# Optimization experiments

Measured on AMD Instinct MI355X. Metric: run time of the kernel, lower is better.

## Reference

```python
import jax, jax.numpy as jnp
import numpy as np

EMBED = 1024
HEADS = 16
HEAD_DIM = EMBED // HEADS

def setup_inputs() -> dict:
    key = jax.random.key(0)
    ks = jax.random.split(key, 12)
    N, L, E = 4, 2048, EMBED
    s = 1.0 / np.sqrt(E)
    return {
        "values": jax.random.normal(ks[0], (N, L, E), jnp.float32),
        "keys": jax.random.normal(ks[1], (N, L, E), jnp.float32),
        "query": jax.random.normal(ks[2], (N, L, E), jnp.float32),
        "mask": jnp.ones((N, 1, 1, L), jnp.int32),
        "Wv": jax.random.normal(ks[3], (E, E), jnp.float32) * s,
        "bv": jnp.zeros((E,), jnp.float32),
        "Wk": jax.random.normal(ks[4], (E, E), jnp.float32) * s,
        "bk": jnp.zeros((E,), jnp.float32),
        "Wq": jax.random.normal(ks[5], (E, E), jnp.float32) * s,
        "bq": jnp.zeros((E,), jnp.float32),
        "Wo": jax.random.normal(ks[6], (E, E), jnp.float32) * s,
        "bo": jnp.zeros((E,), jnp.float32),
    }

def reference(values, keys, query, mask, Wv, bv, Wk, bk, Wq, bq, Wo, bo):
    N, L, E = values.shape
    H, D = HEADS, HEAD_DIM
    v = (values @ Wv + bv).reshape(N, L, H, D)
    k = (keys @ Wk + bk).reshape(N, L, H, D)
    q = (query @ Wq + bq).reshape(N, L, H, D)
    # energy: [N, H, Lq, Lk]
    energy = jnp.einsum('nqhd,nkhd->nhqk', q, k)
    energy = jnp.where(mask == 0, jnp.float32(-1e20), energy)
    attn = jax.nn.softmax(energy / np.sqrt(D), axis=3)
    out = jnp.einsum('nhqk,nkhd->nqhd', attn, v).reshape(N, L, E)
    return out @ Wo + bo
```

## Files before the change

kernel.cpp:

```cpp
#include <hip/hip_runtime.h>
#include <hip/hip_bf16.h>


#define N_B 4
#define L_S 2048
#define E_D 1024
#define H_N 16
#define D_H 64

typedef __attribute__((ext_vector_type(8))) short short8;
typedef __attribute__((ext_vector_type(8))) unsigned short ushort8;
typedef __attribute__((ext_vector_type(4))) unsigned short ushort4v;
typedef __attribute__((ext_vector_type(4))) float f32x4;

#define EXP2F(x) __builtin_amdgcn_exp2f(x)

__device__ __forceinline__ unsigned short f2b(float f) {
    unsigned int u = __builtin_bit_cast(unsigned int, f);
    u += 0x7fffu + ((u >> 16) & 1u);
    return (unsigned short)(u >> 16);
}

__device__ __forceinline__ void gload16(const void* g, void* l) {
    __builtin_amdgcn_global_load_lds(
        (const __attribute__((address_space(1))) void*)g,
        (__attribute__((address_space(3))) void*)l, 16, 0, 0);
}

__global__ __launch_bounds__(256) void cvt3_kernel(const float* __restrict__ v,
                                                   const float* __restrict__ k,
                                                   const float* __restrict__ q,
                                                   unsigned short* __restrict__ out) {
    int z = blockIdx.y;
    const float* in = (z == 0) ? v : ((z == 1) ? k : q);
    unsigned short* o = out + (size_t)z * (8u << 20);
    size_t i = (size_t)blockIdx.x * 256 + threadIdx.x;
    const float* p = in + i * 8;
    ushort8 ov;
#pragma unroll
    for (int j = 0; j < 8; j++) ov[j] = f2b(p[j]);
    *(ushort8*)(o + i * 8) = ov;
}

__global__ __launch_bounds__(256) void wtrans4_kernel(const float* __restrict__ W0,
                                                      const float* __restrict__ W1,
                                                      const float* __restrict__ W2,
                                                      const float* __restrict__ W3,
                                                      unsigned short* __restrict__ WtBase) {
    __shared__ float t[64][65];
    int z = blockIdx.z;
    const float* W = (z == 0) ? W0 : ((z == 1) ? W1 : ((z == 2) ? W2 : W3));
    unsigned short* Wt = WtBase + (size_t)z * (1u << 20);
    int bx = blockIdx.x, by = blockIdx.y;
    int tx = threadIdx.x;
    int r0 = tx >> 4;
    int c4 = (tx & 15) << 2;
#pragma unroll
    for (int rr = 0; rr < 64; rr += 16) {
        const float* src = W + (size_t)(by * 64 + rr + r0) * E_D + bx * 64 + c4;
        float4 v = *(const float4*)src;
        t[rr + r0][c4 + 0] = v.x; t[rr + r0][c4 + 1] = v.y;
        t[rr + r0][c4 + 2] = v.z; t[rr + r0][c4 + 3] = v.w;
    }
    __syncthreads();
#pragma unroll
    for (int rr = 0; rr < 64; rr += 16) {
        int nrow = bx * 64 + rr + r0;
        ushort4v o;
#pragma unroll
        for (int j = 0; j < 4; j++) o[j] = f2b(t[c4 + j][rr + r0]);
        *(ushort4v*)(Wt + (size_t)nrow * E_D + by * 64 + c4) = o;
    }
}

template <int OUTF32>
__device__ __forceinline__ void gemm_body(
    const unsigned short* __restrict__ A, const unsigned short* __restrict__ Bt,
    const float* __restrict__ bias, void* __restrict__ C,
    int K, int Nc, float scale,
    unsigned short* As, unsigned short* Bs, int n0, int m0) {
    int lane = threadIdx.x & 63, wave = threadIdx.x >> 6;
    int wr = (wave >> 1) * 64, wc = (wave & 1) * 64;
    f32x4 acc[4][4] = {};
    int nk = K >> 6;
    for (int kt = 0; kt < nk; ++kt) {
#pragma unroll
        for (int i = 0; i < 4; i++) {
            int c = (i * 4 + wave) * 64 + lane;
            int row = c >> 3;
            int csw = (c & 7) ^ (row & 7);
            gload16(A + (size_t)(m0 + row) * K + kt * 64 + csw * 8,
                    As + (size_t)(i * 4 + wave) * 512);
            gload16(Bt + (size_t)(n0 + row) * K + kt * 64 + csw * 8,
                    Bs + (size_t)(i * 4 + wave) * 512);
        }
        __syncthreads();
#pragma unroll
        for (int ks = 0; ks < 2; ++ks) {
            short8 a[4], b[4];
#pragma unroll
            for (int mi = 0; mi < 4; mi++) {
                int row = wr + mi * 16 + (lane & 15);
                int ch = (ks * 4 + (lane >> 4)) ^ (row & 7);
                a[mi] = *(const short8*)(As + row * 64 + ch * 8);
            }
#pragma unroll
            for (int ni = 0; ni < 4; ni++) {
                int col = wc + ni * 16 + (lane & 15);
                int ch = (ks * 4 + (lane >> 4)) ^ (col & 7);
                b[ni] = *(const short8*)(Bs + col * 64 + ch * 8);
            }
#pragma unroll
            for (int mi = 0; mi < 4; mi++)
#pragma unroll
                for (int ni = 0; ni < 4; ni++)
                    acc[mi][ni] = __builtin_amdgcn_mfma_f32_16x16x32_bf16(
                        a[mi], b[ni], acc[mi][ni], 0, 0, 0);
        }
        __syncthreads();
    }
#pragma unroll
    for (int ni = 0; ni < 4; ni++) {
        int col = n0 + wc + ni * 16 + (lane & 15);
        float bb = bias[col];
#pragma unroll
        for (int mi = 0; mi < 4; mi++) {
            int rbase = m0 + wr + mi * 16 + (lane >> 4) * 4;
#pragma unroll
            for (int r = 0; r < 4; r++) {
                float v = (acc[mi][ni][r] + bb) * scale;
                if (OUTF32)
                    ((float*)C)[(size_t)(rbase + r) * Nc + col] = v;
                else
                    ((unsigned short*)C)[(size_t)(rbase + r) * Nc + col] = f2b(v);
            }
        }
    }
}

template <int OUTF32>
__global__ __launch_bounds__(256, 3) void gemm_kernel(
    const unsigned short* __restrict__ A, const unsigned short* __restrict__ Bt,
    const float* __restrict__ bias, void* __restrict__ C,
    int M, int K, int Nc, float scale) {
    __shared__ unsigned short As[128 * 64];
    __shared__ unsigned short Bs[128 * 64];
    gemm_body<OUTF32>(A, Bt, bias, C, K, Nc, scale, As, Bs,
                      blockIdx.x * 128, blockIdx.y * 128);
}

__global__ __launch_bounds__(256, 3) void gemm3_kernel(
    const unsigned short* __restrict__ Abase, const unsigned short* __restrict__ Wtbase,
    const float* __restrict__ bv, const float* __restrict__ bk, const float* __restrict__ bq,
    unsigned short* __restrict__ Cbase, float qscale) {
    __shared__ unsigned short As[128 * 64];
    __shared__ unsigned short Bs[128 * 64];
    int z = blockIdx.z;
    const unsigned short* A  = Abase + (size_t)z * (8u << 20);
    const unsigned short* Bt = Wtbase + (size_t)z * (1u << 20);
    const float* bias = (z == 0) ? bv : ((z == 1) ? bk : bq);
    unsigned short* C = Cbase + (size_t)z * (8u << 20);
    float scale = (z == 2) ? qscale : 1.0f;
    gemm_body<0>(A, Bt, bias, C, E_D, E_D, scale, As, Bs,
                 blockIdx.x * 128, blockIdx.y * 128);
}

__global__ __launch_bounds__(256) void vtrans_kernel(const unsigned short* __restrict__ v,
                                                     unsigned short* __restrict__ vt) {
    __shared__ unsigned short t[64 * 65];
    int l0 = blockIdx.x * 64, h = blockIdx.y, n = blockIdx.z;
    int tx = threadIdx.x;
    int r = tx >> 3;
    int c8 = (tx & 7) << 3;
#pragma unroll
    for (int rr = 0; rr < 64; rr += 32) {
        ushort8 val = *(const ushort8*)(v + (size_t)(n * L_S + l0 + rr + r) * E_D + h * 64 + c8);
#pragma unroll
        for (int j = 0; j < 8; j++) t[(rr + r) * 65 + c8 + j] = val[j];
    }
    __syncthreads();
#pragma unroll
    for (int rr = 0; rr < 64; rr += 32) {
        int d = rr + r;
        ushort8 o;
#pragma unroll
        for (int j = 0; j < 8; j++) o[j] = t[(c8 + j) * 65 + d];
        *(ushort8*)(vt + (size_t)((n * H_N + h) * D_H + d) * L_S + l0 + c8) = o;
    }
}

__global__ __launch_bounds__(512, 4) void attn_kernel(
    const unsigned short* __restrict__ qb, const unsigned short* __restrict__ kb,
    const unsigned short* __restrict__ vt, const int* __restrict__ mask,
    unsigned short* __restrict__ aout) {
    __shared__ unsigned short Ks[2][64 * 64];
    __shared__ unsigned short Vs[2][64 * 64];
    __shared__ unsigned short Ps[8][32 * 64];
    __shared__ alignas(8) unsigned char okb[256];
    int lane = threadIdx.x & 63, wave = threadIdx.x >> 6;
    int g = lane >> 4, c = lane & 15;
    const float SHIFT = 20.0f;

    int bid = blockIdx.x;
    int xcd = bid & 7, idx = bid >> 3;
    int grp = xcd * 8 + (idx >> 3);
    int q0 = (idx & 7) * 256;
    int h = grp & 15;
    int n = grp >> 4;

    const unsigned short* qptr  = qb + (size_t)n * L_S * E_D + h * 64;
    const unsigned short* kbase = kb + (size_t)n * L_S * E_D + h * 64;
    const unsigned short* vbase = vt + (size_t)(n * H_N + h) * D_H * L_S;
    const int* mbase = mask + n * L_S;

    if (threadIdx.x < 256) {
        int t8 = threadIdx.x * 8;
        int4 ma = *(const int4*)(mbase + t8);
        int4 mb = *(const int4*)(mbase + t8 + 4);
        int ok = (ma.x != 0) & (ma.y != 0) & (ma.z != 0) & (ma.w != 0) &
                 (mb.x != 0) & (mb.y != 0) & (mb.z != 0) & (mb.w != 0);
        okb[threadIdx.x] = (unsigned char)ok;
    }
    unsigned short* Qs = &Ps[0][0];
#pragma unroll
    for (int i = 0; i < 4; i++) {
        int ci = i * 8 + wave;
        int cc = ci * 64 + lane;
        int row = cc >> 3, csw = (cc & 7) ^ (row & 7);
        gload16(qptr + (size_t)(q0 + row) * E_D + csw * 8, Qs + (size_t)ci * 512);
    }
    {
        int cc = wave * 64 + lane;
        int row = cc >> 3, csw = (cc & 7) ^ (row & 7);
        gload16(kbase + (size_t)row * E_D + csw * 8, Ks[0] + wave * 512);
        gload16(vbase + (size_t)row * L_S + csw * 8, Vs[0] + wave * 512);
    }
    __syncthreads();

    short8 qf[2][2];
#pragma unroll
    for (int m = 0; m < 2; m++)
#pragma unroll
        for (int kd = 0; kd < 2; kd++) {
            int row = wave * 32 + m * 16 + c;
            int ch = (kd * 4 + g) ^ (row & 7);
            qf[m][kd] = *(const short8*)(Qs + row * 64 + ch * 8);
        }

    f32x4 o[2][4] = {};
    float lrun[2] = {0.f, 0.f};
    unsigned short* pw = &Ps[wave][0];

    const int NT = L_S / 64;
    for (int kt = 0; kt < NT; ++kt) {
        int cur = kt & 1;
        if (kt + 1 < NT) {
            int cc = wave * 64 + lane;
            int row = cc >> 3, csw = (cc & 7) ^ (row & 7);
            gload16(kbase + (size_t)((kt + 1) * 64 + row) * E_D + csw * 8,
                    Ks[cur ^ 1] + wave * 512);
            gload16(vbase + (size_t)row * L_S + (kt + 1) * 64 + csw * 8,
                    Vs[cur ^ 1] + wave * 512);
            asm volatile("s_waitcnt vmcnt(2)" ::: "memory");
        } else {
            asm volatile("s_waitcnt vmcnt(0)" ::: "memory");
        }
        __builtin_amdgcn_s_barrier();
        __builtin_amdgcn_sched_barrier(0);

        const unsigned short* KsC = Ks[cur];
        const unsigned short* VsC = Vs[cur];

        f32x4 sT[2][4] = {};
        __builtin_amdgcn_s_setprio(1);
#pragma unroll
        for (int kd = 0; kd < 2; kd++)
#pragma unroll
            for (int kg = 0; kg < 4; kg++) {
                int krow = kg * 16 + c;
                int ch = (kd * 4 + g) ^ (krow & 7);
                short8 kf = *(const short8*)(KsC + krow * 64 + ch * 8);
                sT[0][kg] = __builtin_amdgcn_mfma_f32_16x16x32_bf16(kf, qf[0][kd], sT[0][kg], 0, 0, 0);
                sT[1][kg] = __builtin_amdgcn_mfma_f32_16x16x32_bf16(kf, qf[1][kd], sT[1][kg], 0, 0, 0);
            }
        __builtin_amdgcn_s_setprio(0);

        uint2 fl = *(const uint2*)&okb[kt * 8];
        bool dense = ((fl.x & fl.y) == 0x01010101u);
        if (!dense) {
#pragma unroll
            for (int kg = 0; kg < 4; kg++) {
                int4 mv = *(const int4*)(mbase + kt * 64 + kg * 16 + g * 4);
                float m0 = mv.x ? 0.f : -1e30f;
                float m1 = mv.y ? 0.f : -1e30f;
                float m2 = mv.z ? 0.f : -1e30f;
                float m3 = mv.w ? 0.f : -1e30f;
                sT[0][kg][0] += m0; sT[1][kg][0] += m0;
                sT[0][kg][1] += m1; sT[1][kg][1] += m1;
                sT[0][kg][2] += m2; sT[1][kg][2] += m2;
                sT[0][kg][3] += m3; sT[1][kg][3] += m3;
            }
        }
#pragma unroll
        for (int m = 0; m < 2; m++) {
            float ps = 0.f;
            int prow = m * 16 + c;
#pragma unroll
            for (int kg = 0; kg < 4; kg++) {
                float p0 = EXP2F(sT[m][kg][0] - SHIFT);
                float p1 = EXP2F(sT[m][kg][1] - SHIFT);
                float p2 = EXP2F(sT[m][kg][2] - SHIFT);
                float p3 = EXP2F(sT[m][kg][3] - SHIFT);
                ps += (p0 + p1) + (p2 + p3);
                unsigned int w0, w1;
                asm("v_cvt_pk_bf16_f32 %0, %1, %2" : "=v"(w0) : "v"(p0), "v"(p1));
                asm("v_cvt_pk_bf16_f32 %0, %1, %2" : "=v"(w1) : "v"(p2), "v"(p3));
                int c16 = kg * 2 + (g >> 1);
                int off = prow * 64 + ((c16 ^ (prow & 7)) << 3) + ((g & 1) << 2);
                uint2 wv; wv.x = w0; wv.y = w1;
                *(uint2*)(pw + off) = wv;
            }
            ps += __shfl_xor(ps, 16);
            ps += __shfl_xor(ps, 32);
            lrun[m] += ps;
        }
        __builtin_amdgcn_s_setprio(1);
#pragma unroll
        for (int kk = 0; kk < 2; kk++) {
            short8 pb[2];
#pragma unroll
            for (int m = 0; m < 2; m++) {
                int prow = m * 16 + c;
                int ch = (kk * 4 + g) ^ (prow & 7);
                pb[m] = *(const short8*)(pw + prow * 64 + ch * 8);
            }
#pragma unroll
            for (int dg = 0; dg < 4; dg++) {
                int drow = dg * 16 + c;
                int ch = (kk * 4 + g) ^ (drow & 7);
                short8 vb = *(const short8*)(VsC + drow * 64 + ch * 8);
                o[0][dg] = __builtin_amdgcn_mfma_f32_16x16x32_bf16(vb, pb[0], o[0][dg], 0, 0, 0);
                o[1][dg] = __builtin_amdgcn_mfma_f32_16x16x32_bf16(vb, pb[1], o[1][dg], 0, 0, 0);
            }
        }
        __builtin_amdgcn_s_setprio(0);
        asm volatile("s_waitcnt lgkmcnt(0)" ::: "memory");
        __builtin_amdgcn_s_barrier();
    }
#pragma unroll
    for (int m = 0; m < 2; m++) {
        float inv = 1.f / lrun[m];
        int row = q0 + wave * 32 + m * 16 + c;
#pragma unroll
        for (int dg = 0; dg < 4; dg++) {
            ushort4v ov;
#pragma unroll
            for (int r = 0; r < 4; r++) ov[r] = f2b(o[m][dg][r] * inv);
            *(ushort4v*)(aout + (size_t)(n * L_S + row) * E_D + h * 64 + dg * 16 + g * 4) = ov;
        }
    }
}

extern "C" void kernel_launch(void* const* d_in, const int* in_sizes, int n_in,
                              void* d_out, int out_size, void* d_ws, size_t ws_size,
                              hipStream_t stream) {
    const float* values = (const float*)d_in[0];
    const float* keys   = (const float*)d_in[1];
    const float* query  = (const float*)d_in[2];
    const int*   mask   = (const int*)d_in[3];
    const float* Wv = (const float*)d_in[4];  const float* bv = (const float*)d_in[5];
    const float* Wk = (const float*)d_in[6];  const float* bk = (const float*)d_in[7];
    const float* Wq = (const float*)d_in[8];  const float* bq = (const float*)d_in[9];
    const float* Wo = (const float*)d_in[10]; const float* bo = (const float*)d_in[11];
    float* out = (float*)d_out;
    char* ws = (char*)d_ws;
    const size_t MB = 1ull << 20;
    unsigned short* xv  = (unsigned short*)(ws + 0 * MB);
    unsigned short* wtv = (unsigned short*)(ws + 48 * MB);
    unsigned short* wto = (unsigned short*)(ws + 54 * MB);
    unsigned short* vbf = (unsigned short*)(ws + 56 * MB);
    unsigned short* kbf = (unsigned short*)(ws + 72 * MB);
    unsigned short* qbf = (unsigned short*)(ws + 88 * MB);
    unsigned short* vT  = (unsigned short*)(ws + 0 * MB);
    unsigned short* aob = (unsigned short*)(ws + 16 * MB);

    const float QS = 0.125f * 1.4426950408889634f;

    cvt3_kernel<<<dim3(4096, 3), 256, 0, stream>>>(values, keys, query, xv);
    wtrans4_kernel<<<dim3(16, 16, 4), 256, 0, stream>>>(Wv, Wk, Wq, Wo, wtv);
    gemm3_kernel<<<dim3(E_D / 128, (N_B * L_S) / 128, 3), 256, 0, stream>>>(
        xv, wtv, bv, bk, bq, vbf, QS);
    vtrans_kernel<<<dim3(32, 16, 4), 256, 0, stream>>>(vbf, vT);
    attn_kernel<<<dim3(512), 512, 0, stream>>>(qbf, kbf, vT, mask, aob);
    gemm_kernel<1><<<dim3(E_D / 128, (N_B * L_S) / 128), 256, 0, stream>>>(
        aob, wto, bo, out, N_B * L_S, E_D, E_D, 1.0f);
}
```

Measured before the change: 217.8 us.

## Fuse V transpose into V-projection GEMM epilogue via LDS staging

```diff
diff --git a/kernel.cpp b/kernel.cpp
--- a/kernel.cpp
+++ b/kernel.cpp
@@ -73,7 +73,7 @@
     }
 }
 
-template <int OUTF32>
+template <int OUTMODE>
 __device__ __forceinline__ void gemm_body(
     const unsigned short* __restrict__ A, const unsigned short* __restrict__ Bt,
     const float* __restrict__ bias, void* __restrict__ C,
@@ -119,6 +119,42 @@
         }
         __syncthreads();
     }
+    if (OUTMODE == 2) {
+        int g = lane >> 4, c = lane & 15;
+        unsigned short* tb = As + wave * 4096;
+#pragma unroll
+        for (int ni = 0; ni < 4; ni++) {
+            int cl = ni * 16 + c;
+            float bb = bias[n0 + wc + cl];
+#pragma unroll
+            for (int mi = 0; mi < 4; mi++) {
+#pragma unroll
+                for (int r = 0; r < 4; r++) {
+                    int rl = mi * 16 + g * 4 + r;
+                    tb[rl * 64 + (((cl >> 3) ^ (rl & 7)) << 3) + (cl & 7)] =
+                        f2b((acc[mi][ni][r] + bb) * scale);
+                }
+            }
+        }
+        int mrow = m0 + wr;
+        int n = mrow >> 11;
+        int l0 = mrow & 2047;
+        int h = (n0 + wc) >> 6;
+        unsigned short* vt = (unsigned short*)C;
+#pragma unroll
+        for (int i = 0; i < 8; i++) {
+            int d = i * 8 + (lane >> 3);
+            int lc = (lane & 7) * 8;
+            ushort8 ov;
+#pragma unroll
+            for (int j = 0; j < 8; j++) {
+                int rl = lc + j;
+                ov[j] = tb[rl * 64 + (((d >> 3) ^ (rl & 7)) << 3) + (d & 7)];
+            }
+            *(ushort8*)(vt + (size_t)((n * H_N + h) * D_H + d) * L_S + l0 + lc) = ov;
+        }
+        return;
+    }
 #pragma unroll
     for (int ni = 0; ni < 4; ni++) {
         int col = n0 + wc + ni * 16 + (lane & 15);
@@ -129,7 +165,7 @@
 #pragma unroll
             for (int r = 0; r < 4; r++) {
                 float v = (acc[mi][ni][r] + bb) * scale;
-                if (OUTF32)
+                if (OUTMODE == 1)
                     ((float*)C)[(size_t)(rbase + r) * Nc + col] = v;
                 else
                     ((unsigned short*)C)[(size_t)(rbase + r) * Nc + col] = f2b(v);
@@ -138,54 +174,32 @@
     }
 }
 
-template <int OUTF32>
-__global__ __launch_bounds__(256, 3) void gemm_kernel(
+template <int OUTMODE>
+__global__ __launch_bounds__(256, 2) void gemm_kernel(
     const unsigned short* __restrict__ A, const unsigned short* __restrict__ Bt,
     const float* __restrict__ bias, void* __restrict__ C,
     int M, int K, int Nc, float scale) {
-    __shared__ unsigned short As[128 * 64];
-    __shared__ unsigned short Bs[128 * 64];
-    gemm_body<OUTF32>(A, Bt, bias, C, K, Nc, scale, As, Bs,
-                      blockIdx.x * 128, blockIdx.y * 128);
-}
-
-__global__ __launch_bounds__(256, 3) void gemm3_kernel(
+    __shared__ unsigned short SMEM[2][128 * 64];
+    gemm_body<OUTMODE>(A, Bt, bias, C, K, Nc, scale, SMEM[0], SMEM[1],
+                       blockIdx.x * 128, blockIdx.y * 128);
+}
+
+__global__ __launch_bounds__(256, 2) void gemm3_kernel(
     const unsigned short* __restrict__ Abase, const unsigned short* __restrict__ Wtbase,
     const float* __restrict__ bv, const float* __restrict__ bk, const float* __restrict__ bq,
-    unsigned short* __restrict__ Cbase, float qscale) {
-    __shared__ unsigned short As[128 * 64];
-    __shared__ unsigned short Bs[128 * 64];
+    unsigned short* __restrict__ vT, unsigned short* __restrict__ kbf,
+    unsigned short* __restrict__ qbf, float qscale) {
+    __shared__ unsigned short SMEM[2][128 * 64];
     int z = blockIdx.z;
     const unsigned short* A  = Abase + (size_t)z * (8u << 20);
     const unsigned short* Bt = Wtbase + (size_t)z * (1u << 20);
-    const float* bias = (z == 0) ? bv : ((z == 1) ? bk : bq);
-    unsigned short* C = Cbase + (size_t)z * (8u << 20);
-    float scale = (z == 2) ? qscale : 1.0f;
-    gemm_body<0>(A, Bt, bias, C, E_D, E_D, scale, As, Bs,
-                 blockIdx.x * 128, blockIdx.y * 128);
-}
-
-__global__ __launch_bounds__(256) void vtrans_kernel(const unsigned short* __restrict__ v,
-                                                     unsigned short* __restrict__ vt) {
-    __shared__ unsigned short t[64 * 65];
-    int l0 = blockIdx.x * 64, h = blockIdx.y, n = blockIdx.z;
-    int tx = threadIdx.x;
-    int r = tx >> 3;
-    int c8 = (tx & 7) << 3;
-#pragma unroll
-    for (int rr = 0; rr < 64; rr += 32) {
-        ushort8 val = *(const ushort8*)(v + (size_t)(n * L_S + l0 + rr + r) * E_D + h * 64 + c8);
-#pragma unroll
-        for (int j = 0; j < 8; j++) t[(rr + r) * 65 + c8 + j] = val[j];
-    }
-    __syncthreads();
-#pragma unroll
-    for (int rr = 0; rr < 64; rr += 32) {
-        int d = rr + r;
-        ushort8 o;
-#pragma unroll
-        for (int j = 0; j < 8; j++) o[j] = t[(c8 + j) * 65 + d];
-        *(ushort8*)(vt + (size_t)((n * H_N + h) * D_H + d) * L_S + l0 + c8) = o;
+    int n0 = blockIdx.x * 128, m0 = blockIdx.y * 128;
+    if (z == 0) {
+        gemm_body<2>(A, Bt, bv, vT, E_D, E_D, 1.0f, SMEM[0], SMEM[1], n0, m0);
+    } else if (z == 1) {
+        gemm_body<0>(A, Bt, bk, kbf, E_D, E_D, 1.0f, SMEM[0], SMEM[1], n0, m0);
+    } else {
+        gemm_body<0>(A, Bt, bq, qbf, E_D, E_D, qscale, SMEM[0], SMEM[1], n0, m0);
     }
 }
 
@@ -378,10 +392,9 @@
     unsigned short* xv  = (unsigned short*)(ws + 0 * MB);
     unsigned short* wtv = (unsigned short*)(ws + 48 * MB);
     unsigned short* wto = (unsigned short*)(ws + 54 * MB);
-    unsigned short* vbf = (unsigned short*)(ws + 56 * MB);
+    unsigned short* vT  = (unsigned short*)(ws + 56 * MB);
     unsigned short* kbf = (unsigned short*)(ws + 72 * MB);
     unsigned short* qbf = (unsigned short*)(ws + 88 * MB);
-    unsigned short* vT  = (unsigned short*)(ws + 0 * MB);
     unsigned short* aob = (unsigned short*)(ws + 16 * MB);
 
     const float QS = 0.125f * 1.4426950408889634f;
@@ -389,8 +402,7 @@
     cvt3_kernel<<<dim3(4096, 3), 256, 0, stream>>>(values, keys, query, xv);
     wtrans4_kernel<<<dim3(16, 16, 4), 256, 0, stream>>>(Wv, Wk, Wq, Wo, wtv);
     gemm3_kernel<<<dim3(E_D / 128, (N_B * L_S) / 128, 3), 256, 0, stream>>>(
-        xv, wtv, bv, bk, bq, vbf, QS);
-    vtrans_kernel<<<dim3(32, 16, 4), 256, 0, stream>>>(vbf, vT);
+        xv, wtv, bv, bk, bq, vT, kbf, qbf, QS);
     attn_kernel<<<dim3(512), 512, 0, stream>>>(qbf, kbf, vT, mask, aob);
     gemm_kernel<1><<<dim3(E_D / 128, (N_B * L_S) / 128), 256, 0, stream>>>(
         aob, wto, bo, out, N_B * L_S, E_D, E_D, 1.0f);
```

Result: faster. 212.1 us (-2.6%).
